# Kernel tuning notes

Hardware: AMD Instinct MI355X
Metric: run time of the kernel (lower is better)

Reference implementation:

```python
import jax, jax.numpy as jnp
import numpy as np

K = 9          # neighbors kept after dilation
DILATION = 2   # top-k runs with K*DILATION then strided slice
EPS = 1e-12    # F.normalize eps


def setup_inputs() -> dict:
    key = jax.random.key(0)
    # x: [B, C, N, 1] feature map over N points with C channels
    x = jax.random.normal(key, (2, 64, 8192, 1), dtype=jnp.float32)
    return {"x": x}


def reference(x):
    k_total = K * DILATION
    # L2-normalize along channel dim (F.normalize(x, p=2, dim=1))
    norm = jnp.sqrt(jnp.sum(x * x, axis=1, keepdims=True))
    xn = x / jnp.maximum(norm, EPS)
    # [B, C, N, 1] -> [B, N, C]
    pts = jnp.transpose(jnp.squeeze(xn, -1), (0, 2, 1))
    B, N, _ = pts.shape
    # pairwise squared distances: ||xi||^2 - 2 xi.xj + ||xj||^2  -> [B, N, N]
    sq = jnp.sum(pts * pts, axis=-1, keepdims=True)            # [B, N, 1]
    dist = sq - 2.0 * jnp.einsum('bnc,bmc->bnm', pts, pts) + jnp.swapaxes(sq, 1, 2)
    # k nearest = top-k of negated distance (matches torch.topk(-dist, k))
    _, nn_idx = jax.lax.top_k(-dist, k_total)                  # [B, N, k_total] int32
    center_idx = jnp.broadcast_to(jnp.arange(N, dtype=nn_idx.dtype)[None, :, None],
                                  (B, N, k_total))
    edge_index = jnp.stack([nn_idx, center_idx], axis=0)       # [2, B, N, k_total]
    # dilation (non-stochastic path): strided slice over neighbor dim
    return edge_index[:, :, :, ::DILATION]                     # [2, B, N, K]
```

## Files before the change

### kernel.cpp

```cpp
#include <hip/hip_runtime.h>


#define NPTS  8192
#define CHN   64
#define NB    2
#define KF    18
#define KC    8
#define KM    20
#define KOUT  9
#define NPART 4
#define TPB   32

typedef unsigned u32;
typedef unsigned short u16;
typedef unsigned long long u64;
typedef __attribute__((ext_vector_type(4))) unsigned u32x4;
typedef __attribute__((ext_vector_type(8))) short bf16x8;
typedef __attribute__((ext_vector_type(4))) float f32x4;

__device__ __forceinline__ u32 umin32(u32 a, u32 b) { return a < b ? a : b; }

__device__ __forceinline__ u32 mono32(float f) {
  const u32 u = __float_as_uint(f);
  const u32 s = (u32)((int)u >> 31);
  return u ^ (s | 0x80000000u);
}

__device__ __forceinline__ u32 med3u(u32 a, u32 b, u32 c) {
  u32 r;
  asm("v_med3_u32 %0, %1, %2, %3" : "=v"(r) : "v"(a), "v"(b), "v"(c));
  return r;
}

template <int KK>
__device__ __forceinline__ void insmm(u32 key, u32 (&d)[KK]) {
#pragma unroll
  for (int k = KK - 1; k >= 1; --k) d[k] = med3u(d[k - 1], d[k], key);
  d[0] = umin32(d[0], key);
}

template <int KK>
__device__ __forceinline__ void ins64(u64 key, u64 (&d)[KK]) {
  if (key < d[KK - 1]) {
#pragma unroll
    for (int k = KK - 1; k >= 1; --k) {
      const bool up = d[k - 1] > key;
      const bool here = (!up) && (d[k] > key);
      d[k] = up ? d[k - 1] : (here ? key : d[k]);
    }
    if (d[0] > key) d[0] = key;
  }
}

__device__ __forceinline__ void gload_lds16(const u32* g, u32* l) {
  __builtin_amdgcn_global_load_lds(
      (const __attribute__((address_space(1))) u32*)g,
      (__attribute__((address_space(3))) u32*)l, 16, 0, 0);
}

__device__ __forceinline__ void np_normalize(const float* __restrict__ xb,
                                             float (&v)[CHN]) {
  float ss = 0.f;
#pragma unroll
  for (int c = 0; c < CHN; ++c) {
    v[c] = xb[(size_t)c * NPTS];
    ss = __fadd_rn(ss, __fmul_rn(v[c], v[c]));
  }
  const float den = fmaxf(__fsqrt_rn(ss), 1e-12f);
#pragma unroll
  for (int c = 0; c < CHN; ++c) v[c] = __fdiv_rn(v[c], den);
}

__global__ __launch_bounds__(128) void prep_kernel(
    const float* __restrict__ x, u32* __restrict__ hib, u32* __restrict__ lob,
    float* __restrict__ sq) {
  const int b = blockIdx.x >> 6;
  const int n = ((blockIdx.x & 63) << 7) + threadIdx.x;
  const int g = (b << 13) + n;
  float v[CHN];
  np_normalize(x + (size_t)b * CHN * NPTS + n, v);
  float r[8];
#pragma unroll
  for (int j = 0; j < 8; ++j) r[j] = __fmul_rn(v[j], v[j]);
#pragma unroll
  for (int blk = 1; blk < 8; ++blk)
#pragma unroll
    for (int j = 0; j < 8; ++j)
      r[j] = __fadd_rn(r[j], __fmul_rn(v[8 * blk + j], v[8 * blk + j]));
  const float t0 = __fadd_rn(r[0], r[1]);
  const float t1 = __fadd_rn(r[2], r[3]);
  const float t2 = __fadd_rn(r[4], r[5]);
  const float t3 = __fadd_rn(r[6], r[7]);
  sq[g] = __fadd_rn(__fadd_rn(t0, t1), __fadd_rn(t2, t3));
  u32* hd = hib + (size_t)g * 32;
  u32* ld = lob + (size_t)g * 32;
  const int key = n & 7;
#pragma unroll
  for (int q = 0; q < 8; ++q) {
    u32 h[4], l[4];
#pragma unroll
    for (int p2 = 0; p2 < 4; ++p2) {
      const float a = v[8 * q + 2 * p2];
      const float c = v[8 * q + 2 * p2 + 1];
      const u32 ba = __float_as_uint(a), bc = __float_as_uint(c);
      const float la = a - __uint_as_float(ba & 0xffff0000u);
      const float lc = c - __uint_as_float(bc & 0xffff0000u);
      h[p2] = __builtin_amdgcn_perm(bc, ba, 0x07060302u);
      l[p2] = __builtin_amdgcn_perm(__float_as_uint(lc), __float_as_uint(la),
                                    0x07060302u);
    }
    const int pq = (q ^ key) << 2;
    *(u32x4*)(hd + pq) = (u32x4){h[0], h[1], h[2], h[3]};
    *(u32x4*)(ld + pq) = (u32x4){l[0], l[1], l[2], l[3]};
  }
}

__global__ __launch_bounds__(128) void prep2_kernel(
    const float* __restrict__ x, float* __restrict__ pts) {
  const int b = blockIdx.x >> 6;
  const int n = ((blockIdx.x & 63) << 7) + threadIdx.x;
  float v[CHN];
  np_normalize(x + (size_t)b * CHN * NPTS + n, v);
  float4* dst = (float4*)(pts + (size_t)((b << 13) + n) * CHN);
#pragma unroll
  for (int u = 0; u < 16; ++u)
    dst[u] = make_float4(v[4 * u], v[4 * u + 1], v[4 * u + 2], v[4 * u + 3]);
}

__global__ __launch_bounds__(256, 2) void knn_part_kernel(
    const u32* __restrict__ hib, const u32* __restrict__ lob,
    const float* __restrict__ sq, u16* __restrict__ cand) {
  __shared__ __align__(16) u32 pw[4][2][2048];

  const int tid = threadIdx.x;
  const int vb = ((blockIdx.x & 7) << 7) + (blockIdx.x >> 3);
  const int part = vb >> 8;
  const int w = vb & 255;
  const int b = w >> 7;
  const int qbase = (w & 127) << 6;
  const int t_lo = part << 5;
  const u32* __restrict__ hb_ = hib + ((size_t)b << 18);
  const u32* __restrict__ lb_ = lob + ((size_t)b << 18);
  const float* __restrict__ sqb = sq + (b << 13);

  const int lane = tid & 63, wid = tid >> 6;
  const int qoff = (wid & 1) << 5;
  const int moff = (wid >> 1) << 5;
  const int l15 = lane & 15;
  const int h4 = lane >> 4;
  const int sw = l15 & 7;

  const int lofs = lane << 2;
#define STAGE(BUF, TILE)                                                     \
  {                                                                          \
    const u32* sH_ = hb_ + ((size_t)(TILE) << 11) + (moff << 5);             \
    const u32* sL_ = lb_ + ((size_t)(TILE) << 11) + (moff << 5);             \
    u32* bp_ = &pw[wid][(BUF)][0];                                           \
    gload_lds16(sH_ + lofs, bp_ + lofs);                                     \
    gload_lds16(sH_ + 256 + lofs, bp_ + 256 + lofs);                         \
    gload_lds16(sH_ + 512 + lofs, bp_ + 512 + lofs);                         \
    gload_lds16(sH_ + 768 + lofs, bp_ + 768 + lofs);                         \
    gload_lds16(sL_ + lofs, bp_ + 1024 + lofs);                              \
    gload_lds16(sL_ + 256 + lofs, bp_ + 1280 + lofs);                        \
    gload_lds16(sL_ + 512 + lofs, bp_ + 1536 + lofs);                        \
    gload_lds16(sL_ + 768 + lofs, bp_ + 1792 + lofs);                        \
  }

  STAGE(0, t_lo)
  float sqn0 = sqb[(t_lo << 6) + moff + l15];
  float sqn1 = sqb[(t_lo << 6) + moff + 16 + l15];

  bf16x8 ah[2][2], al[2][2];
#pragma unroll
  for (int g = 0; g < 2; ++g)
#pragma unroll
    for (int s = 0; s < 2; ++s) {
      const int row = qbase + qoff + (g << 4) + l15;
      const int off = row * 32 + ((((s << 2) + h4) ^ sw) << 2);
      u32x4 hv = *(const u32x4*)(hb_ + off);
      u32x4 lv = *(const u32x4*)(lb_ + off);
      hv.x ^= 0x80008000u; hv.y ^= 0x80008000u;
      hv.z ^= 0x80008000u; hv.w ^= 0x80008000u;
      lv.x ^= 0x80008000u; lv.y ^= 0x80008000u;
      lv.z ^= 0x80008000u; lv.w ^= 0x80008000u;
      ah[g][s] = __builtin_bit_cast(bf16x8, hv);
      al[g][s] = __builtin_bit_cast(bf16x8, lv);
    }
  asm volatile("s_waitcnt vmcnt(0)" ::: "memory");
  __builtin_amdgcn_sched_barrier(0);

  u32 d[2][4][KC];
#pragma unroll
  for (int g = 0; g < 2; ++g)
#pragma unroll
    for (int i = 0; i < 4; ++i)
#pragma unroll
      for (int k = 0; k < KC; ++k) d[g][i][k] = 0xffffffffu;

  for (int tau = 0; tau < TPB; ++tau) {
    const int cur = tau & 1;
    const float sq0 = sqn0, sq1 = sqn1;
    if (tau + 1 < TPB) {
      STAGE(cur ^ 1, t_lo + tau + 1)
      sqn0 = sqb[((t_lo + tau + 1) << 6) + moff + l15];
      sqn1 = sqb[((t_lo + tau + 1) << 6) + moff + 16 + l15];
      asm volatile("s_waitcnt vmcnt(10)" ::: "memory");
    } else {
      asm volatile("s_waitcnt vmcnt(0)" ::: "memory");
    }
    __builtin_amdgcn_sched_barrier(0);

    const u32* ppc = &pw[wid][cur][0];
#pragma unroll
    for (int f = 0; f < 2; ++f) {
      const float sqm = ((f ? sq1 : sq0) + 2.f) * 0.5f;
      const int rloc = (f << 4) + l15;
      f32x4 acc[2];
      acc[0] = (f32x4){sqm, sqm, sqm, sqm};
      acc[1] = acc[0];
#pragma unroll
      for (int s = 0; s < 2; ++s) {
        const u32* hp = ppc + rloc * 32 + ((((s << 2) + h4) ^ sw) << 2);
        const bf16x8 bh = __builtin_bit_cast(bf16x8, *(const u32x4*)hp);
        const bf16x8 bl = __builtin_bit_cast(bf16x8, *(const u32x4*)(hp + 1024));
        acc[0] = __builtin_amdgcn_mfma_f32_16x16x32_bf16(ah[0][s], bh, acc[0], 0, 0, 0);
        acc[1] = __builtin_amdgcn_mfma_f32_16x16x32_bf16(ah[1][s], bh, acc[1], 0, 0, 0);
        acc[0] = __builtin_amdgcn_mfma_f32_16x16x32_bf16(al[0][s], bh, acc[0], 0, 0, 0);
        acc[1] = __builtin_amdgcn_mfma_f32_16x16x32_bf16(al[1][s], bh, acc[1], 0, 0, 0);
        acc[0] = __builtin_amdgcn_mfma_f32_16x16x32_bf16(ah[0][s], bl, acc[0], 0, 0, 0);
        acc[1] = __builtin_amdgcn_mfma_f32_16x16x32_bf16(ah[1][s], bl, acc[1], 0, 0, 0);
      }
      const u32 lidx = (u32)((tau << 6) + moff + rloc);
#pragma unroll
      for (int g = 0; g < 2; ++g)
#pragma unroll
        for (int i = 0; i < 4; ++i) {
          const u32 keyv = (__float_as_uint(acc[g][i]) & 0xfffff000u) | lidx;
          insmm<KC>(keyv, d[g][i]);
        }
    }
  }
#undef STAGE
  __syncthreads();

  u32* mg = &pw[0][0][0];
  const int stream = ((wid >> 1) << 4) + l15;
  const int rcb = ((wid & 1) << 4) + (h4 << 2);
#pragma unroll
  for (int chunk = 0; chunk < 2; ++chunk) {
#pragma unroll
    for (int i = 0; i < 4; ++i) {
      u32* wr = mg + ((rcb + i) * 32 + stream) * 8;
      u32x4 a, c;
      a.x = d[chunk][i][0]; a.y = d[chunk][i][1];
      a.z = d[chunk][i][2]; a.w = d[chunk][i][3];
      c.x = d[chunk][i][4]; c.y = d[chunk][i][5];
      c.z = d[chunk][i][6]; c.w = d[chunk][i][7];
      *(u32x4*)wr = a;
      *(u32x4*)(wr + 4) = c;
    }
    __syncthreads();
    {
      const int rowc = tid >> 3, oct = tid & 7;
      u32* base = mg + rowc * 256 + oct * 32;
      u32 m1[14];
#pragma unroll
      for (int k = 0; k < 14; ++k) m1[k] = 0xffffffffu;
#pragma unroll
      for (int j = 0; j < 8; ++j) {
        const u32x4 k4 = *(const u32x4*)(base + (j << 2));
        insmm<14>(k4.x, m1);
        insmm<14>(k4.y, m1);
        insmm<14>(k4.z, m1);
        insmm<14>(k4.w, m1);
      }
#pragma unroll
      for (int k = 0; k < 14; ++k) base[k] = m1[k];
    }
    __syncthreads();
    if (tid < 64) {
      const int rowc = tid >> 1, half = tid & 1;
      u32* rb = mg + rowc * 256 + half * 128;
      u32 m2[KM];
#pragma unroll
      for (int k = 0; k < KM; ++k) m2[k] = 0xffffffffu;
#pragma unroll
      for (int o = 0; o < 4; ++o) {
        const u32* p = rb + o * 32;
        for (int j = 0; j < 14; ++j) insmm<KM>(p[j], m2);
      }
#pragma unroll
      for (int k = 0; k < KM; ++k) rb[k] = m2[k];
    }
    __syncthreads();
    if (tid < 32) {
      u32 m3[KM];
#pragma unroll
      for (int k = 0; k < KM; ++k) m3[k] = 0xffffffffu;
      const u32* p0 = mg + tid * 256;
      for (int j = 0; j < KM; ++j) insmm<KM>(p0[j], m3);
      const u32* p1 = mg + tid * 256 + 128;
      for (int j = 0; j < KM; ++j) insmm<KM>(p1[j], m3);
      const int row = ((tid >> 4) << 5) + (chunk << 4) + (tid & 15);
      const int rg = (b << 13) + qbase + row;
      u16* cw = cand + (size_t)rg * (NPART * KM) + part * KM;
#pragma unroll
      for (int k = 0; k < KM; ++k)
        cw[k] = (u16)((part << 11) + (m3[k] & 0xfffu));
    }
    __syncthreads();
  }
}

__global__ __launch_bounds__(512) void finalize_kernel(
    const float* __restrict__ pts, const float* __restrict__ sq,
    const u16* __restrict__ cand, int* __restrict__ out) {
  __shared__ u64 ex[64 * 81];
  __shared__ u64 hf[128 * 19];
  const int tid = threadIdx.x;
  const int rl = tid >> 3, sub = tid & 7;
  const int row = (blockIdx.x << 6) + rl;
  const int b = row >> 13;
  const float sqn = sq[row];
  const float* __restrict__ qrow = pts + ((size_t)row << 6);
  const float* __restrict__ sqb = sq + (b << 13);
  const u16* __restrict__ cr = cand + (size_t)row * 80 + sub * 10;
  u64* exw = ex + rl * 81 + sub * 10;
#pragma unroll 2
  for (int j = 0; j < 10; ++j) {
    const int ix = cr[j];
    const float* __restrict__ pv = pts + ((size_t)((b << 13) + ix) << 6);
    float dot = 0.f;
#pragma unroll
    for (int c = 0; c < CHN; ++c)
      dot = __fadd_rn(dot, __fmul_rn(qrow[c], pv[c]));
    const float dist =
        __fadd_rn(__fsub_rn(sqn, __fmul_rn(2.0f, dot)), sqb[ix]);
    exw[j] = ((u64)mono32(dist) << 32) | (u32)ix;
  }
  __syncthreads();
  if (tid < 128) {
    const int r2 = tid >> 1, hv = tid & 1;
    u64 m18[KF];
#pragma unroll
    for (int k = 0; k < KF; ++k) m18[k] = ~0ull;
    const u64* p = ex + r2 * 81 + hv * 40;
    for (int j = 0; j < 40; ++j) ins64<KF>(p[j], m18);
    u64* wr = hf + tid * 19;
#pragma unroll
    for (int k = 0; k < KF; ++k) wr[k] = m18[k];
  }
  __syncthreads();
  if (tid < 64) {
    u64 m18[KF];
#pragma unroll
    for (int k = 0; k < KF; ++k) m18[k] = ~0ull;
    const u64* p0 = hf + (tid << 1) * 19;
    const u64* p1 = hf + ((tid << 1) + 1) * 19;
    for (int j = 0; j < KF; ++j) ins64<KF>(p0[j], m18);
    for (int j = 0; j < KF; ++j) ins64<KF>(p1[j], m18);
    const int row2 = (blockIdx.x << 6) + tid;
    int* o0 = out + (size_t)row2 * KOUT;
    int* o1 = o0 + NB * NPTS * KOUT;
#pragma unroll
    for (int k = 0; k < KOUT; ++k) {
      o0[k] = (int)(m18[2 * k] & 0xffffffffu);
      o1[k] = row2 & 8191;
    }
  }
}

extern "C" void kernel_launch(void* const* d_in, const int* in_sizes, int n_in,
                              void* d_out, int out_size, void* d_ws, size_t ws_size,
                              hipStream_t stream) {
  const float* x = (const float*)d_in[0];
  u32* hib = (u32*)d_ws;
  u32* lob = hib + (size_t)NB * NPTS * 32;
  float* pts = (float*)d_ws;
  float* sqg = (float*)(hib + (size_t)NB * NPTS * 64);
  u16* cand = (u16*)(sqg + NB * NPTS);
  int* out = (int*)d_out;
  prep_kernel<<<dim3(128), dim3(128), 0, stream>>>(x, hib, lob, sqg);
  knn_part_kernel<<<dim3(1024), dim3(256), 0, stream>>>(hib, lob, sqg, cand);
  prep2_kernel<<<dim3(128), dim3(128), 0, stream>>>(x, pts);
  finalize_kernel<<<dim3(256), dim3(512), 0, stream>>>(pts, sqg, cand, out);
}
```

Before: 235.1 us.

## Drop prep2 kernel, rebuild fp32 points from split bf16 halves in finalize

Prep now also writes the low 16 bits of each float into a third swizzled buffer, so finalize can rebuild the exact normalized fp32 vectors from the high and low halves. That removes the separate prep2 kernel, which re-normalized the input and wrote a full fp32 point array. The candidate count per partition also drops from 20 to 16, shrinking the finalize exact-distance and merge work. The smaller candidate set risks missing true neighbors near the top-18 boundary.

```diff
diff --git a/kernel.cpp b/kernel.cpp
--- a/kernel.cpp
+++ b/kernel.cpp
@@ -6,7 +6,7 @@
 #define NB    2
 #define KF    18
 #define KC    8
-#define KM    20
+#define KM    16
 #define KOUT  9
 #define NPART 4
 #define TPB   32
@@ -73,7 +73,7 @@
 
 __global__ __launch_bounds__(128) void prep_kernel(
     const float* __restrict__ x, u32* __restrict__ hib, u32* __restrict__ lob,
-    float* __restrict__ sq) {
+    u32* __restrict__ w16b, float* __restrict__ sq) {
   const int b = blockIdx.x >> 6;
   const int n = ((blockIdx.x & 63) << 7) + threadIdx.x;
   const int g = (b << 13) + n;
@@ -94,10 +94,11 @@
   sq[g] = __fadd_rn(__fadd_rn(t0, t1), __fadd_rn(t2, t3));
   u32* hd = hib + (size_t)g * 32;
   u32* ld = lob + (size_t)g * 32;
+  u32* wd = w16b + (size_t)g * 32;
   const int key = n & 7;
 #pragma unroll
   for (int q = 0; q < 8; ++q) {
-    u32 h[4], l[4];
+    u32 h[4], l[4], w[4];
 #pragma unroll
     for (int p2 = 0; p2 < 4; ++p2) {
       const float a = v[8 * q + 2 * p2];
@@ -108,23 +109,13 @@
       h[p2] = __builtin_amdgcn_perm(bc, ba, 0x07060302u);
       l[p2] = __builtin_amdgcn_perm(__float_as_uint(lc), __float_as_uint(la),
                                     0x07060302u);
+      w[p2] = __builtin_amdgcn_perm(bc, ba, 0x05040100u);
     }
     const int pq = (q ^ key) << 2;
     *(u32x4*)(hd + pq) = (u32x4){h[0], h[1], h[2], h[3]};
     *(u32x4*)(ld + pq) = (u32x4){l[0], l[1], l[2], l[3]};
-  }
-}
-
-__global__ __launch_bounds__(128) void prep2_kernel(
-    const float* __restrict__ x, float* __restrict__ pts) {
-  const int b = blockIdx.x >> 6;
-  const int n = ((blockIdx.x & 63) << 7) + threadIdx.x;
-  float v[CHN];
-  np_normalize(x + (size_t)b * CHN * NPTS + n, v);
-  float4* dst = (float4*)(pts + (size_t)((b << 13) + n) * CHN);
-#pragma unroll
-  for (int u = 0; u < 16; ++u)
-    dst[u] = make_float4(v[4 * u], v[4 * u + 1], v[4 * u + 2], v[4 * u + 3]);
+    *(u32x4*)(wd + pq) = (u32x4){w[0], w[1], w[2], w[3]};
+  }
 }
 
 __global__ __launch_bounds__(256, 2) void knn_part_kernel(
@@ -149,8 +140,8 @@
   const int l15 = lane & 15;
   const int h4 = lane >> 4;
   const int sw = l15 & 7;
-
   const int lofs = lane << 2;
+
 #define STAGE(BUF, TILE)                                                     \
   {                                                                          \
     const u32* sH_ = hb_ + ((size_t)(TILE) << 11) + (moff << 5);             \
@@ -313,27 +304,64 @@
 }
 
 __global__ __launch_bounds__(512) void finalize_kernel(
-    const float* __restrict__ pts, const float* __restrict__ sq,
-    const u16* __restrict__ cand, int* __restrict__ out) {
-  __shared__ u64 ex[64 * 81];
+    const u32* __restrict__ hib, const u32* __restrict__ w16b,
+    const float* __restrict__ sq, const u16* __restrict__ cand,
+    int* __restrict__ out) {
+  __shared__ u64 ex[64 * 66];
   __shared__ u64 hf[128 * 19];
   const int tid = threadIdx.x;
   const int rl = tid >> 3, sub = tid & 7;
   const int row = (blockIdx.x << 6) + rl;
   const int b = row >> 13;
+  const int n = row & 8191;
   const float sqn = sq[row];
-  const float* __restrict__ qrow = pts + ((size_t)row << 6);
   const float* __restrict__ sqb = sq + (b << 13);
-  const u16* __restrict__ cr = cand + (size_t)row * 80 + sub * 10;
-  u64* exw = ex + rl * 81 + sub * 10;
-#pragma unroll 2
-  for (int j = 0; j < 10; ++j) {
+  const u32* __restrict__ hb_ = hib + ((size_t)b << 18);
+  const u32* __restrict__ wb_ = w16b + ((size_t)b << 18);
+  float vq[CHN];
+  {
+    const u32* hq = hb_ + ((size_t)n << 5);
+    const u32* wq = wb_ + ((size_t)n << 5);
+    const int key = n & 7;
+#pragma unroll
+    for (int q = 0; q < 8; ++q) {
+      const int pq = (q ^ key) << 2;
+      const u32x4 hw = *(const u32x4*)(hq + pq);
+      const u32x4 ww = *(const u32x4*)(wq + pq);
+      const u32 hv[4] = {hw.x, hw.y, hw.z, hw.w};
+      const u32 wv[4] = {ww.x, ww.y, ww.z, ww.w};
+#pragma unroll
+      for (int p2 = 0; p2 < 4; ++p2) {
+        vq[8 * q + 2 * p2] =
+            __uint_as_float((hv[p2] << 16) | (wv[p2] & 0xffffu));
+        vq[8 * q + 2 * p2 + 1] =
+            __uint_as_float((hv[p2] & 0xffff0000u) | (wv[p2] >> 16));
+      }
+    }
+  }
+  const u16* __restrict__ cr = cand + (size_t)row * 64 + sub * 8;
+  u64* exw = ex + rl * 66 + sub * 8;
+  for (int j = 0; j < 8; ++j) {
     const int ix = cr[j];
-    const float* __restrict__ pv = pts + ((size_t)((b << 13) + ix) << 6);
+    const u32* hp = hb_ + ((size_t)ix << 5);
+    const u32* wp = wb_ + ((size_t)ix << 5);
+    const int key = ix & 7;
     float dot = 0.f;
 #pragma unroll
-    for (int c = 0; c < CHN; ++c)
-      dot = __fadd_rn(dot, __fmul_rn(qrow[c], pv[c]));
+    for (int q = 0; q < 8; ++q) {
+      const int pq = (q ^ key) << 2;
+      const u32x4 hw = *(const u32x4*)(hp + pq);
+      const u32x4 ww = *(const u32x4*)(wp + pq);
+      const u32 hv[4] = {hw.x, hw.y, hw.z, hw.w};
+      const u32 wv[4] = {ww.x, ww.y, ww.z, ww.w};
+#pragma unroll
+      for (int p2 = 0; p2 < 4; ++p2) {
+        const float a = __uint_as_float((hv[p2] << 16) | (wv[p2] & 0xffffu));
+        const float c = __uint_as_float((hv[p2] & 0xffff0000u) | (wv[p2] >> 16));
+        dot = __fadd_rn(dot, __fmul_rn(vq[8 * q + 2 * p2], a));
+        dot = __fadd_rn(dot, __fmul_rn(vq[8 * q + 2 * p2 + 1], c));
+      }
+    }
     const float dist =
         __fadd_rn(__fsub_rn(sqn, __fmul_rn(2.0f, dot)), sqb[ix]);
     exw[j] = ((u64)mono32(dist) << 32) | (u32)ix;
@@ -344,8 +372,8 @@
     u64 m18[KF];
 #pragma unroll
     for (int k = 0; k < KF; ++k) m18[k] = ~0ull;
-    const u64* p = ex + r2 * 81 + hv * 40;
-    for (int j = 0; j < 40; ++j) ins64<KF>(p[j], m18);
+    const u64* p = ex + r2 * 66 + hv * 32;
+    for (int j = 0; j < 32; ++j) ins64<KF>(p[j], m18);
     u64* wr = hf + tid * 19;
 #pragma unroll
     for (int k = 0; k < KF; ++k) wr[k] = m18[k];
@@ -376,12 +404,11 @@
   const float* x = (const float*)d_in[0];
   u32* hib = (u32*)d_ws;
   u32* lob = hib + (size_t)NB * NPTS * 32;
-  float* pts = (float*)d_ws;
-  float* sqg = (float*)(hib + (size_t)NB * NPTS * 64);
+  u32* w16b = lob + (size_t)NB * NPTS * 32;
+  float* sqg = (float*)(w16b + (size_t)NB * NPTS * 32);
   u16* cand = (u16*)(sqg + NB * NPTS);
   int* out = (int*)d_out;
-  prep_kernel<<<dim3(128), dim3(128), 0, stream>>>(x, hib, lob, sqg);
+  prep_kernel<<<dim3(128), dim3(128), 0, stream>>>(x, hib, lob, w16b, sqg);
   knn_part_kernel<<<dim3(1024), dim3(256), 0, stream>>>(hib, lob, sqg, cand);
-  prep2_kernel<<<dim3(128), dim3(128), 0, stream>>>(x, pts);
-  finalize_kernel<<<dim3(256), dim3(512), 0, stream>>>(pts, sqg, cand, out);
-}
+  finalize_kernel<<<dim3(256), dim3(512), 0, stream>>>(hib, w16b, sqg, cand, out);
+}
```

New measurement: 210.1 us. -10.6%, faster.
